# Optimization experiments

Hardware: AMD Instinct MI355X
Metric: run time of the kernel (lower is better)

Reference implementation:

```python
import jax, jax.numpy as jnp
import numpy as np

N0, N1, N2, N3 = 1_000_000, 200_000, 20_000, 2_048
E0, E1, E2 = 2_000_000, 200_000, 20_480
IN, HID, OUT = 128, 256, 47


def setup_inputs() -> dict:
    key = jax.random.key(0)
    ks = jax.random.split(key, 16)
    d = {}
    d["x"] = jax.random.normal(ks[0], (N0, IN), dtype=jnp.float32)
    # block edge lists (src index into layer-input nodes, dst into layer-output nodes)
    d["src0"] = jax.random.randint(ks[1], (E0,), 0, N0)
    d["dst0"] = jax.random.randint(ks[2], (E0,), 0, N1)
    d["src1"] = jax.random.randint(ks[3], (E1,), 0, N1)
    d["dst1"] = jax.random.randint(ks[4], (E1,), 0, N2)
    d["src2"] = jax.random.randint(ks[5], (E2,), 0, N2)
    d["dst2"] = jax.random.randint(ks[6], (E2,), 0, N3)
    # SAGEConv params: fc_self / fc_neigh (bias-free) + shared bias
    def lin(k, fi, fo):
        return jax.random.normal(k, (fi, fo), dtype=jnp.float32) / np.sqrt(fi).astype(np.float32)
    d["W_self0"], d["W_neigh0"], d["b0"] = lin(ks[7], IN, HID), lin(ks[8], IN, HID), jnp.zeros((HID,), jnp.float32)
    d["W_self1"], d["W_neigh1"], d["b1"] = lin(ks[9], HID, HID), lin(ks[10], HID, HID), jnp.zeros((HID,), jnp.float32)
    d["W_self2"], d["W_neigh2"], d["b2"] = lin(ks[11], HID, OUT), lin(ks[12], HID, OUT), jnp.zeros((OUT,), jnp.float32)
    return d


def _sage_layer(h, src, dst, n_dst, W_self, W_neigh, b):
    # gather messages from src nodes, mean-reduce onto dst nodes
    msg = h[src]                                   # [E, d_in]
    agg = jax.ops.segment_sum(msg, dst, num_segments=n_dst)
    deg = jax.ops.segment_sum(jnp.ones((src.shape[0],), h.dtype), dst, num_segments=n_dst)
    h_neigh = agg / jnp.maximum(deg, 1.0)[:, None]
    h_dst = h[:n_dst]                              # DGL block convention: dst = first n_dst src nodes
    return h_dst @ W_self + h_neigh @ W_neigh + b


def reference(x, src0, dst0, src1, dst1, src2, dst2,
              W_self0, W_neigh0, b0, W_self1, W_neigh1, b1, W_self2, W_neigh2, b2):
    h = _sage_layer(x, src0, dst0, N1, W_self0, W_neigh0, b0)
    h = jax.nn.relu(h)  # dropout is identity in eval mode
    h = _sage_layer(h, src1, dst1, N2, W_self1, W_neigh1, b1)
    h = jax.nn.relu(h)
    h = _sage_layer(h, src2, dst2, N3, W_self2, W_neigh2, b2)
    return h
```

## Files before the change

### kernel.cpp

```cpp
#include <hip/hip_runtime.h>

#define N0_ 1000000
#define N1_ 200000
#define N2_ 20000
#define N3_ 2048
#define E0_ 2000000
#define E1_ 200000
#define E2_ 20480
#define IN_ 128
#define HID_ 256
#define OUT_ 47

typedef unsigned short u16;
typedef unsigned int u32;
typedef __attribute__((ext_vector_type(8))) short b16x8;
typedef __attribute__((ext_vector_type(4))) float f32x4;
typedef __attribute__((ext_vector_type(4))) u16 u16x4;
typedef __attribute__((ext_vector_type(8))) u16 u16x8;

__device__ __forceinline__ u16 f2b(float f) {
  u32 u = __builtin_bit_cast(u32, f);
  return (u16)((u + 0x7FFFu + ((u >> 16) & 1u)) >> 16);
}
__device__ __forceinline__ float b2f(u16 b) {
  return __builtin_bit_cast(float, (u32)b << 16);
}

static constexpr size_t OFF_CNT  = 0;
static constexpr size_t OFF_CUR  = 200064;
static constexpr size_t OFF_RPTR = 400128;
static constexpr size_t OFF_BSUM = 600192;
static constexpr size_t OFF_EIDS = 600320;
static constexpr size_t OFF_BT0  = 2600320;
static constexpr size_t OFF_BT1  = 2633088;
static constexpr size_t OFF_HN0  = 2698624;
static constexpr size_t OFF_H1   = 15498624;
static constexpr size_t OFF_HN1  = 41098624;
static constexpr size_t OFF_H2   = 43658624;
static constexpr size_t OFF_HN2  = 46218624;

__global__ __launch_bounds__(256) void hist_kernel(const int* __restrict__ dst,
                                                   int* __restrict__ cnt, int nE) {
  int e = blockIdx.x * 256 + threadIdx.x;
  if (e < nE) atomicAdd(&cnt[dst[e]], 1);
}

__global__ __launch_bounds__(256) void scan_local(const int* __restrict__ in,
                                                  int* __restrict__ out,
                                                  int* __restrict__ bsum, int n) {
  __shared__ int s[256];
  const int b = blockIdx.x, t = threadIdx.x;
  const int base = b * 2048 + t * 8;
  int v[8];
  int sum = 0;
#pragma unroll
  for (int i = 0; i < 8; i++) {
    int idx = base + i;
    int x = (idx < n) ? in[idx] : 0;
    v[i] = sum;
    sum += x;
  }
  s[t] = sum;
  __syncthreads();
  for (int off = 1; off < 256; off <<= 1) {
    int x = 0;
    if (t >= off) x = s[t - off];
    __syncthreads();
    if (t >= off) s[t] += x;
    __syncthreads();
  }
  const int texcl = s[t] - sum;
#pragma unroll
  for (int i = 0; i < 8; i++) {
    int idx = base + i;
    if (idx < n) out[idx] = texcl + v[i];
  }
  if (t == 255) bsum[b] = s[255];
}

__global__ __launch_bounds__(256) void scan_add(int* __restrict__ rptr,
                                                const int* __restrict__ bsum,
                                                int n, int E) {
  const int b = blockIdx.x, t = threadIdx.x;
  int add = 0;
  for (int i = 0; i < b; i++) add += bsum[i];
  const int base = b * 2048 + t * 8;
#pragma unroll
  for (int i = 0; i < 8; i++) {
    int idx = base + i;
    if (idx < n) rptr[idx] += add;
  }
  if (b == 0 && t == 0) rptr[n] = E;
}

__global__ __launch_bounds__(256) void csr_fill(const int* __restrict__ src,
                                                const int* __restrict__ dst,
                                                const int* __restrict__ rptr,
                                                int* __restrict__ cursor,
                                                int* __restrict__ eids, int nE) {
  int e = blockIdx.x * 256 + threadIdx.x;
  if (e >= nE) return;
  int d = dst[e];
  int pos = rptr[d] + atomicAdd(&cursor[d], 1);
  eids[pos] = src[e];
}

__global__ __launch_bounds__(256) void pack_w(const float* __restrict__ Ws,
                                              const float* __restrict__ Wn,
                                              u16* __restrict__ Bt, int KS, int KT) {
  int t = blockIdx.x * 256 + threadIdx.x;
  if (t >= 256 * KT) return;
  int n = t & 255, k = t >> 8;
  float v = (k < KS) ? Ws[(size_t)k * 256 + n] : Wn[(size_t)(k - KS) * 256 + n];
  Bt[(size_t)n * KT + k] = f2b(v);
}

__global__ __launch_bounds__(256) void agg0(const float* __restrict__ h,
                                            const int* __restrict__ eids,
                                            const int* __restrict__ rptr,
                                            u16* __restrict__ out, int M) {
  int wid = (blockIdx.x * 256 + threadIdx.x) >> 6;
  int lane = threadIdx.x & 63;
  if (wid >= M) return;
  const int beg = rptr[wid], end = rptr[wid + 1];
  const int half = lane >> 5;
  const int col = (lane & 31) * 4;
  float a0 = 0.f, a1 = 0.f, a2 = 0.f, a3 = 0.f;
  for (int i = beg; i < end; i += 16) {
    int ids[8];
#pragma unroll
    for (int j = 0; j < 8; j++) {
      int idx = i + 2 * j + half;
      idx = idx < end ? idx : end - 1;
      ids[j] = eids[idx];
    }
    float4 v[8];
#pragma unroll
    for (int j = 0; j < 8; j++)
      v[j] = *reinterpret_cast<const float4*>(&h[(size_t)ids[j] * IN_ + col]);
#pragma unroll
    for (int j = 0; j < 8; j++) {
      if (i + 2 * j + half < end) {
        a0 += v[j].x; a1 += v[j].y; a2 += v[j].z; a3 += v[j].w;
      }
    }
  }
  a0 += __shfl_xor(a0, 32, 64);
  a1 += __shfl_xor(a1, 32, 64);
  a2 += __shfl_xor(a2, 32, 64);
  a3 += __shfl_xor(a3, 32, 64);
  if (half == 0) {
    float inv = 1.0f / fmaxf((float)(end - beg), 1.0f);
    u16x4 o;
    o[0] = f2b(a0 * inv); o[1] = f2b(a1 * inv);
    o[2] = f2b(a2 * inv); o[3] = f2b(a3 * inv);
    *reinterpret_cast<u16x4*>(&out[(size_t)wid * IN_ + col]) = o;
  }
}

__global__ __launch_bounds__(256) void agg1(const u16* __restrict__ h,
                                            const int* __restrict__ eids,
                                            const int* __restrict__ rptr,
                                            u16* __restrict__ out, int M) {
  int wid = (blockIdx.x * 256 + threadIdx.x) >> 6;
  int lane = threadIdx.x & 63;
  if (wid >= M) return;
  const int beg = rptr[wid], end = rptr[wid + 1];
  const int half = lane >> 5;
  const int col = (lane & 31) * 8;
  float a[8];
#pragma unroll
  for (int j = 0; j < 8; j++) a[j] = 0.f;
  for (int i = beg; i < end; i += 16) {
    int ids[8];
#pragma unroll
    for (int j = 0; j < 8; j++) {
      int idx = i + 2 * j + half;
      idx = idx < end ? idx : end - 1;
      ids[j] = eids[idx];
    }
    u16x8 v[8];
#pragma unroll
    for (int j = 0; j < 8; j++)
      v[j] = *reinterpret_cast<const u16x8*>(&h[(size_t)ids[j] * HID_ + col]);
#pragma unroll
    for (int j = 0; j < 8; j++) {
      if (i + 2 * j + half < end) {
#pragma unroll
        for (int c = 0; c < 8; c++) a[c] += b2f(v[j][c]);
      }
    }
  }
#pragma unroll
  for (int c = 0; c < 8; c++) a[c] += __shfl_xor(a[c], 32, 64);
  if (half == 0) {
    float inv = 1.0f / fmaxf((float)(end - beg), 1.0f);
    u16x8 o;
#pragma unroll
    for (int c = 0; c < 8; c++) o[c] = f2b(a[c] * inv);
    *reinterpret_cast<u16x8*>(&out[(size_t)wid * HID_ + col]) = o;
  }
}

template <int KSELF, bool A0F32>
__global__ __launch_bounds__(512) void sage_gemm_mfma(
    const void* __restrict__ A0v, const u16* __restrict__ A1,
    const u16* __restrict__ Bt, const float* __restrict__ bias,
    u16* __restrict__ outp, int M) {
  constexpr int KTOT = 2 * KSELF;
  __shared__ u16 As[128 * 64];
  __shared__ u16 Bs[256 * 64];
  const int tid = threadIdx.x;
  const int lane = tid & 63;
  const int w = tid >> 6;
  const int wm = w >> 2;
  const int wn = w & 3;
  const int m0 = blockIdx.x * 128;

  f32x4 acc[4][4];
#pragma unroll
  for (int m = 0; m < 4; m++)
#pragma unroll
    for (int n = 0; n < 4; n++) acc[m][n] = f32x4{0.f, 0.f, 0.f, 0.f};

  for (int kt = 0; kt < KTOT; kt += 64) {
    if (A0F32 && kt < KSELF) {
      const float* A0 = (const float*)A0v;
#pragma unroll
      for (int i = 0; i < 4; i++) {
        int e = tid + i * 512;
        int row = e >> 4;
        int c = (e & 15) * 4;
        int rowg = m0 + row; if (rowg >= M) rowg = M - 1;
        float4 v = *reinterpret_cast<const float4*>(&A0[(size_t)rowg * KSELF + kt + c]);
        u32 p0 = (u32)f2b(v.x) | ((u32)f2b(v.y) << 16);
        u32 p1 = (u32)f2b(v.z) | ((u32)f2b(v.w) << 16);
        int byt = ((row * 64 + c) * 2) ^ ((row & 7) << 4);
        u32* dp = reinterpret_cast<u32*>(reinterpret_cast<char*>(As) + byt);
        dp[0] = p0; dp[1] = p1;
      }
    } else {
      const u16* src; int ksrc;
      if (!A0F32 && kt < KSELF) { src = (const u16*)A0v; ksrc = kt; }
      else                      { src = A1;              ksrc = kt - KSELF; }
#pragma unroll
      for (int i = 0; i < 2; i++) {
        int e = tid + i * 512;
        int row = e >> 3;
        int ch = e & 7;
        int rowg = m0 + row; if (rowg >= M) rowg = M - 1;
        u16x8 v = *reinterpret_cast<const u16x8*>(&src[(size_t)rowg * KSELF + ksrc + ch * 8]);
        int byt = ((row * 64 + ch * 8) * 2) ^ ((row & 7) << 4);
        *reinterpret_cast<u16x8*>(reinterpret_cast<char*>(As) + byt) = v;
      }
    }
#pragma unroll
    for (int i = 0; i < 4; i++) {
      int e = tid + i * 512;
      int n = e >> 3;
      int ch = e & 7;
      u16x8 v = *reinterpret_cast<const u16x8*>(&Bt[(size_t)n * KTOT + kt + ch * 8]);
      int byt = ((n * 64 + ch * 8) * 2) ^ ((n & 7) << 4);
      *reinterpret_cast<u16x8*>(reinterpret_cast<char*>(Bs) + byt) = v;
    }
    __syncthreads();
#pragma unroll
    for (int kk = 0; kk < 64; kk += 32) {
      const int kb = (kk + (lane >> 4) * 8) * 2;
      b16x8 a[4], b[4];
#pragma unroll
      for (int m = 0; m < 4; m++) {
        int row = wm * 64 + m * 16 + (lane & 15);
        int byt = (row * 128 + kb) ^ ((row & 7) << 4);
        a[m] = *reinterpret_cast<const b16x8*>(reinterpret_cast<const char*>(As) + byt);
      }
#pragma unroll
      for (int n = 0; n < 4; n++) {
        int row = wn * 64 + n * 16 + (lane & 15);
        int byt = (row * 128 + kb) ^ ((row & 7) << 4);
        b[n] = *reinterpret_cast<const b16x8*>(reinterpret_cast<const char*>(Bs) + byt);
      }
#pragma unroll
      for (int m = 0; m < 4; m++)
#pragma unroll
        for (int n = 0; n < 4; n++)
          acc[m][n] = __builtin_amdgcn_mfma_f32_16x16x32_bf16(a[m], b[n], acc[m][n], 0, 0, 0);
    }
    __syncthreads();
  }
  float bv[4];
#pragma unroll
  for (int n = 0; n < 4; n++) bv[n] = bias[wn * 64 + n * 16 + (lane & 15)];
#pragma unroll
  for (int m = 0; m < 4; m++) {
    int rowb = m0 + wm * 64 + m * 16 + ((lane >> 4) << 2);
#pragma unroll
    for (int r = 0; r < 4; r++) {
      int row = rowb + r;
      if (row < M) {
#pragma unroll
        for (int n = 0; n < 4; n++) {
          float v = acc[m][n][r] + bv[n];
          v = fmaxf(v, 0.0f);
          outp[(size_t)row * 256 + wn * 64 + n * 16 + (lane & 15)] = f2b(v);
        }
      }
    }
  }
}

__global__ __launch_bounds__(64) void sage_gemm_out(
    const u16* __restrict__ h, const u16* __restrict__ hn,
    const float* __restrict__ Ws, const float* __restrict__ Wn,
    const float* __restrict__ bias, float* __restrict__ out) {
  __shared__ float As[512];
  const int row = blockIdx.x;
  const int t = threadIdx.x;
  u16x4 a = *reinterpret_cast<const u16x4*>(&h[(size_t)row * 256 + t * 4]);
  u16x4 b = *reinterpret_cast<const u16x4*>(&hn[(size_t)row * 256 + t * 4]);
#pragma unroll
  for (int j = 0; j < 4; j++) {
    As[t * 4 + j] = b2f(a[j]);
    As[256 + t * 4 + j] = b2f(b[j]);
  }
  __syncthreads();
  if (t < OUT_) {
    float s = bias[t];
#pragma unroll 8
    for (int k = 0; k < 256; k++) s = fmaf(As[k], Ws[k * 47 + t], s);
#pragma unroll 8
    for (int k = 0; k < 256; k++) s = fmaf(As[256 + k], Wn[k * 47 + t], s);
    out[(size_t)row * 47 + t] = s;
  }
}

static void build_csr(const int* src, const int* dst, int E, int M,
                      int* cnt, int* cursor, int* rptr, int* bsum, int* eids,
                      hipStream_t stream) {
  const int nb = (M + 2047) / 2048;
  hipMemsetAsync(cnt, 0, (size_t)(200064 + M) * 4, stream);
  hist_kernel<<<(E + 255) / 256, 256, 0, stream>>>(dst, cnt, E);
  scan_local<<<nb, 256, 0, stream>>>(cnt, rptr, bsum, M);
  scan_add<<<nb, 256, 0, stream>>>(rptr, bsum, M, E);
  csr_fill<<<(E + 255) / 256, 256, 0, stream>>>(src, dst, rptr, cursor, eids, E);
}

extern "C" void kernel_launch(void* const* d_in, const int* in_sizes, int n_in,
                              void* d_out, int out_size, void* d_ws, size_t ws_size,
                              hipStream_t stream) {
  const float* x      = (const float*)d_in[0];
  const int*   src0   = (const int*)d_in[1];
  const int*   dst0   = (const int*)d_in[2];
  const int*   src1   = (const int*)d_in[3];
  const int*   dst1   = (const int*)d_in[4];
  const int*   src2   = (const int*)d_in[5];
  const int*   dst2   = (const int*)d_in[6];
  const float* Wself0 = (const float*)d_in[7];
  const float* Wneigh0= (const float*)d_in[8];
  const float* b0     = (const float*)d_in[9];
  const float* Wself1 = (const float*)d_in[10];
  const float* Wneigh1= (const float*)d_in[11];
  const float* b1     = (const float*)d_in[12];
  const float* Wself2 = (const float*)d_in[13];
  const float* Wneigh2= (const float*)d_in[14];
  const float* b2     = (const float*)d_in[15];

  int* wsi   = (int*)d_ws;
  int* cnt   = wsi + OFF_CNT;
  int* cursor= wsi + OFF_CUR;
  int* rptr  = wsi + OFF_RPTR;
  int* bsum  = wsi + OFF_BSUM;
  int* eids  = wsi + OFF_EIDS;
  u16* Bt0   = (u16*)(wsi + OFF_BT0);
  u16* Bt1   = (u16*)(wsi + OFF_BT1);
  u16* HN0   = (u16*)(wsi + OFF_HN0);
  u16* H1    = (u16*)(wsi + OFF_H1);
  u16* HN1   = (u16*)(wsi + OFF_HN1);
  u16* H2    = (u16*)(wsi + OFF_H2);
  u16* HN2   = (u16*)(wsi + OFF_HN2);
  float* out = (float*)d_out;

  pack_w<<<(256 * 256 + 255) / 256, 256, 0, stream>>>(Wself0, Wneigh0, Bt0, IN_, 2 * IN_);
  pack_w<<<(256 * 512 + 255) / 256, 256, 0, stream>>>(Wself1, Wneigh1, Bt1, HID_, 2 * HID_);

  build_csr(src0, dst0, E0_, N1_, cnt, cursor, rptr, bsum, eids, stream);
  agg0<<<(N1_ + 3) / 4, 256, 0, stream>>>(x, eids, rptr, HN0, N1_);
  sage_gemm_mfma<IN_, true><<<(N1_ + 127) / 128, 512, 0, stream>>>(x, HN0, Bt0, b0, H1, N1_);

  build_csr(src1, dst1, E1_, N2_, cnt, cursor, rptr, bsum, eids, stream);
  agg1<<<(N2_ + 3) / 4, 256, 0, stream>>>(H1, eids, rptr, HN1, N2_);
  sage_gemm_mfma<HID_, false><<<(N2_ + 127) / 128, 512, 0, stream>>>(H1, HN1, Bt1, b1, H2, N2_);

  build_csr(src2, dst2, E2_, N3_, cnt, cursor, rptr, bsum, eids, stream);
  agg1<<<(N3_ + 3) / 4, 256, 0, stream>>>(H2, eids, rptr, HN2, N3_);
  sage_gemm_out<<<N3_, 64, 0, stream>>>(H2, HN2, Wself2, Wneigh2, b2, out);
}
```

Baseline: 561.4 us.

## Build all three CSRs at once and fuse aggregation into the layer GEMMs

All three layers' destination histograms, prefix scans and CSR fills now run as single combined launches over a concatenated node space, and the weight packing is folded into the histogram kernel. Layer 0's neighbour mean is computed straight into shared memory inside the MFMA GEMM kernel, so the bf16 HN0 buffer is never written to or read back from global memory. The final layer also aggregates neighbours inside the output kernel. This cuts launch count and global round trips, at the cost of a large shared-memory footprint and a serial aggregation phase before the GEMM in fused_sage0, which may lower occupancy and prevent overlap.

```diff
diff --git a/kernel.cpp b/kernel.cpp
--- a/kernel.cpp
+++ b/kernel.cpp
@@ -11,6 +11,9 @@
 #define HID_ 256
 #define OUT_ 47
 
+#define NTOT_ (N1_ + N2_ + N3_)
+#define ETOT_ (E0_ + E1_ + E2_)
+
 typedef unsigned short u16;
 typedef unsigned int u32;
 typedef __attribute__((ext_vector_type(8))) short b16x8;
@@ -27,22 +30,41 @@
 }
 
 static constexpr size_t OFF_CNT  = 0;
-static constexpr size_t OFF_CUR  = 200064;
-static constexpr size_t OFF_RPTR = 400128;
-static constexpr size_t OFF_BSUM = 600192;
-static constexpr size_t OFF_EIDS = 600320;
-static constexpr size_t OFF_BT0  = 2600320;
-static constexpr size_t OFF_BT1  = 2633088;
-static constexpr size_t OFF_HN0  = 2698624;
-static constexpr size_t OFF_H1   = 15498624;
-static constexpr size_t OFF_HN1  = 41098624;
-static constexpr size_t OFF_H2   = 43658624;
-static constexpr size_t OFF_HN2  = 46218624;
-
-__global__ __launch_bounds__(256) void hist_kernel(const int* __restrict__ dst,
-                                                   int* __restrict__ cnt, int nE) {
-  int e = blockIdx.x * 256 + threadIdx.x;
-  if (e < nE) atomicAdd(&cnt[dst[e]], 1);
+static constexpr size_t OFF_CUR  = 222048;
+static constexpr size_t OFF_RPTR = 444096;
+static constexpr size_t OFF_BSUM = 666176;
+static constexpr size_t OFF_EIDS = 666304;
+static constexpr size_t OFF_BT0  = 2886784;
+static constexpr size_t OFF_BT1  = 2919552;
+static constexpr size_t OFF_H1   = 2985088;
+static constexpr size_t OFF_HN1  = 28585088;
+static constexpr size_t OFF_H2   = 31145088;
+
+__global__ __launch_bounds__(256) void prep(
+    const int* __restrict__ dst0, const int* __restrict__ dst1,
+    const int* __restrict__ dst2,
+    const float* __restrict__ Ws0, const float* __restrict__ Wn0,
+    const float* __restrict__ Ws1, const float* __restrict__ Wn1,
+    int* __restrict__ cnt, u16* __restrict__ Bt0, u16* __restrict__ Bt1) {
+  int t = blockIdx.x * 256 + threadIdx.x;
+  if (t < E0_) { atomicAdd(&cnt[dst0[t]], 1); return; }
+  t -= E0_;
+  if (t < E1_) { atomicAdd(&cnt[N1_ + dst1[t]], 1); return; }
+  t -= E1_;
+  if (t < E2_) { atomicAdd(&cnt[N1_ + N2_ + dst2[t]], 1); return; }
+  t -= E2_;
+  if (t < 256 * 256) {
+    int n = t & 255, k = t >> 8;
+    float v = (k < IN_) ? Ws0[(size_t)k * 256 + n] : Wn0[(size_t)(k - IN_) * 256 + n];
+    Bt0[(size_t)n * 256 + k] = f2b(v);
+    return;
+  }
+  t -= 256 * 256;
+  if (t < 256 * 512) {
+    int n = t & 255, k = t >> 8;
+    float v = (k < HID_) ? Ws1[(size_t)k * 256 + n] : Wn1[(size_t)(k - HID_) * 256 + n];
+    Bt1[(size_t)n * 512 + k] = f2b(v);
+  }
 }
 
 __global__ __launch_bounds__(256) void scan_local(const int* __restrict__ in,
@@ -93,68 +115,159 @@
   if (b == 0 && t == 0) rptr[n] = E;
 }
 
-__global__ __launch_bounds__(256) void csr_fill(const int* __restrict__ src,
-                                                const int* __restrict__ dst,
-                                                const int* __restrict__ rptr,
-                                                int* __restrict__ cursor,
-                                                int* __restrict__ eids, int nE) {
+__global__ __launch_bounds__(256) void csr_fill_all(
+    const int* __restrict__ src0, const int* __restrict__ dst0,
+    const int* __restrict__ src1, const int* __restrict__ dst1,
+    const int* __restrict__ src2, const int* __restrict__ dst2,
+    const int* __restrict__ rptr, int* __restrict__ cursor,
+    int* __restrict__ eids) {
   int e = blockIdx.x * 256 + threadIdx.x;
-  if (e >= nE) return;
-  int d = dst[e];
-  int pos = rptr[d] + atomicAdd(&cursor[d], 1);
-  eids[pos] = src[e];
-}
-
-__global__ __launch_bounds__(256) void pack_w(const float* __restrict__ Ws,
-                                              const float* __restrict__ Wn,
-                                              u16* __restrict__ Bt, int KS, int KT) {
-  int t = blockIdx.x * 256 + threadIdx.x;
-  if (t >= 256 * KT) return;
-  int n = t & 255, k = t >> 8;
-  float v = (k < KS) ? Ws[(size_t)k * 256 + n] : Wn[(size_t)(k - KS) * 256 + n];
-  Bt[(size_t)n * KT + k] = f2b(v);
-}
-
-__global__ __launch_bounds__(256) void agg0(const float* __restrict__ h,
-                                            const int* __restrict__ eids,
-                                            const int* __restrict__ rptr,
-                                            u16* __restrict__ out, int M) {
-  int wid = (blockIdx.x * 256 + threadIdx.x) >> 6;
-  int lane = threadIdx.x & 63;
-  if (wid >= M) return;
-  const int beg = rptr[wid], end = rptr[wid + 1];
-  const int half = lane >> 5;
-  const int col = (lane & 31) * 4;
-  float a0 = 0.f, a1 = 0.f, a2 = 0.f, a3 = 0.f;
-  for (int i = beg; i < end; i += 16) {
-    int ids[8];
-#pragma unroll
-    for (int j = 0; j < 8; j++) {
-      int idx = i + 2 * j + half;
-      idx = idx < end ? idx : end - 1;
-      ids[j] = eids[idx];
-    }
-    float4 v[8];
-#pragma unroll
-    for (int j = 0; j < 8; j++)
-      v[j] = *reinterpret_cast<const float4*>(&h[(size_t)ids[j] * IN_ + col]);
-#pragma unroll
-    for (int j = 0; j < 8; j++) {
-      if (i + 2 * j + half < end) {
-        a0 += v[j].x; a1 += v[j].y; a2 += v[j].z; a3 += v[j].w;
-      }
-    }
-  }
-  a0 += __shfl_xor(a0, 32, 64);
-  a1 += __shfl_xor(a1, 32, 64);
-  a2 += __shfl_xor(a2, 32, 64);
-  a3 += __shfl_xor(a3, 32, 64);
-  if (half == 0) {
-    float inv = 1.0f / fmaxf((float)(end - beg), 1.0f);
-    u16x4 o;
-    o[0] = f2b(a0 * inv); o[1] = f2b(a1 * inv);
-    o[2] = f2b(a2 * inv); o[3] = f2b(a3 * inv);
-    *reinterpret_cast<u16x4*>(&out[(size_t)wid * IN_ + col]) = o;
+  int s, b;
+  if (e < E0_) { s = src0[e]; b = dst0[e]; }
+  else if (e < E0_ + E1_) { s = src1[e - E0_]; b = N1_ + dst1[e - E0_]; }
+  else if (e < ETOT_) { s = src2[e - E0_ - E1_]; b = N1_ + N2_ + dst2[e - E0_ - E1_]; }
+  else return;
+  int pos = rptr[b] + atomicAdd(&cursor[b], 1);
+  eids[pos] = s;
+}
+
+__global__ __launch_bounds__(512, 4) void fused_sage0(
+    const float* __restrict__ x, const int* __restrict__ eids,
+    const int* __restrict__ rptr, const u16* __restrict__ Bt,
+    const float* __restrict__ bias, u16* __restrict__ outp, int M) {
+  __shared__ u16 Bs[256 * 64];
+  __shared__ u16 As[128 * 64];
+  __shared__ u16 HN[128 * 128];
+  const int tid = threadIdx.x;
+  const int lane = tid & 63;
+  const int wv = tid >> 6;
+  const int m0 = blockIdx.x * 128;
+
+  {
+    const int half = lane >> 5;
+    const int colf = (lane & 31) * 4;
+    for (int r = 0; r < 16; r++) {
+      const int rl = wv * 16 + r;
+      int rowg = m0 + rl; if (rowg >= M) rowg = M - 1;
+      const int beg = rptr[rowg], end = rptr[rowg + 1];
+      float a0 = 0.f, a1 = 0.f, a2 = 0.f, a3 = 0.f;
+      for (int i = beg; i < end; i += 16) {
+        int ids[8];
+#pragma unroll
+        for (int j = 0; j < 8; j++) {
+          int idx = i + 2 * j + half;
+          idx = idx < end ? idx : end - 1;
+          ids[j] = eids[idx];
+        }
+        float4 v[8];
+#pragma unroll
+        for (int j = 0; j < 8; j++)
+          v[j] = *reinterpret_cast<const float4*>(&x[(size_t)ids[j] * IN_ + colf]);
+#pragma unroll
+        for (int j = 0; j < 8; j++) {
+          if (i + 2 * j + half < end) {
+            a0 += v[j].x; a1 += v[j].y; a2 += v[j].z; a3 += v[j].w;
+          }
+        }
+      }
+      a0 += __shfl_xor(a0, 32, 64);
+      a1 += __shfl_xor(a1, 32, 64);
+      a2 += __shfl_xor(a2, 32, 64);
+      a3 += __shfl_xor(a3, 32, 64);
+      if (half == 0) {
+        float inv = 1.0f / fmaxf((float)(end - beg), 1.0f);
+        u32 p0 = (u32)f2b(a0 * inv) | ((u32)f2b(a1 * inv) << 16);
+        u32 p1 = (u32)f2b(a2 * inv) | ((u32)f2b(a3 * inv) << 16);
+        int byt = (rl * 256 + colf * 2) ^ ((rl & 7) << 4);
+        u32* dp = reinterpret_cast<u32*>(reinterpret_cast<char*>(HN) + byt);
+        dp[0] = p0; dp[1] = p1;
+      }
+    }
+  }
+  __syncthreads();
+
+  const int wm = wv >> 2;
+  const int wn = wv & 3;
+  f32x4 acc[4][4];
+#pragma unroll
+  for (int m = 0; m < 4; m++)
+#pragma unroll
+    for (int n = 0; n < 4; n++) acc[m][n] = f32x4{0.f, 0.f, 0.f, 0.f};
+
+#pragma unroll
+  for (int kt = 0; kt < 256; kt += 64) {
+    if (kt < 128) {
+#pragma unroll
+      for (int i = 0; i < 4; i++) {
+        int e = tid + i * 512;
+        int row = e >> 4;
+        int c = (e & 15) * 4;
+        int rowg = m0 + row; if (rowg >= M) rowg = M - 1;
+        float4 v = *reinterpret_cast<const float4*>(&x[(size_t)rowg * IN_ + kt + c]);
+        u32 p0 = (u32)f2b(v.x) | ((u32)f2b(v.y) << 16);
+        u32 p1 = (u32)f2b(v.z) | ((u32)f2b(v.w) << 16);
+        int byt = ((row * 64 + c) * 2) ^ ((row & 7) << 4);
+        u32* dp = reinterpret_cast<u32*>(reinterpret_cast<char*>(As) + byt);
+        dp[0] = p0; dp[1] = p1;
+      }
+    }
+#pragma unroll
+    for (int i = 0; i < 4; i++) {
+      int e = tid + i * 512;
+      int n = e >> 3;
+      int ch = e & 7;
+      u16x8 v = *reinterpret_cast<const u16x8*>(&Bt[(size_t)n * 256 + kt + ch * 8]);
+      int byt = ((n * 64 + ch * 8) * 2) ^ ((n & 7) << 4);
+      *reinterpret_cast<u16x8*>(reinterpret_cast<char*>(Bs) + byt) = v;
+    }
+    __syncthreads();
+#pragma unroll
+    for (int kk = 0; kk < 64; kk += 32) {
+      const int ksl = kk + (lane >> 4) * 8;
+      b16x8 a[4], b[4];
+#pragma unroll
+      for (int m = 0; m < 4; m++) {
+        int row = wm * 64 + m * 16 + (lane & 15);
+        if (kt < 128) {
+          int byt = (row * 128 + ksl * 2) ^ ((row & 7) << 4);
+          a[m] = *reinterpret_cast<const b16x8*>(reinterpret_cast<const char*>(As) + byt);
+        } else {
+          int byt = (row * 256 + (kt - 128 + ksl) * 2) ^ ((row & 7) << 4);
+          a[m] = *reinterpret_cast<const b16x8*>(reinterpret_cast<const char*>(HN) + byt);
+        }
+      }
+#pragma unroll
+      for (int n = 0; n < 4; n++) {
+        int row = wn * 64 + n * 16 + (lane & 15);
+        int byt = (row * 128 + ksl * 2) ^ ((row & 7) << 4);
+        b[n] = *reinterpret_cast<const b16x8*>(reinterpret_cast<const char*>(Bs) + byt);
+      }
+#pragma unroll
+      for (int m = 0; m < 4; m++)
+#pragma unroll
+        for (int n = 0; n < 4; n++)
+          acc[m][n] = __builtin_amdgcn_mfma_f32_16x16x32_bf16(a[m], b[n], acc[m][n], 0, 0, 0);
+    }
+    __syncthreads();
+  }
+  float bv[4];
+#pragma unroll
+  for (int n = 0; n < 4; n++) bv[n] = bias[wn * 64 + n * 16 + (lane & 15)];
+#pragma unroll
+  for (int m = 0; m < 4; m++) {
+    int rowb = m0 + wm * 64 + m * 16 + ((lane >> 4) << 2);
+#pragma unroll
+    for (int r = 0; r < 4; r++) {
+      int row = rowb + r;
+      if (row < M) {
+#pragma unroll
+        for (int n = 0; n < 4; n++) {
+          float v = acc[m][n][r] + bv[n];
+          v = fmaxf(v, 0.0f);
+          outp[(size_t)row * 256 + wn * 64 + n * 16 + (lane & 15)] = f2b(v);
+        }
+      }
+    }
   }
 }
 
@@ -202,9 +315,9 @@
   }
 }
 
-template <int KSELF, bool A0F32>
+template <int KSELF>
 __global__ __launch_bounds__(512) void sage_gemm_mfma(
-    const void* __restrict__ A0v, const u16* __restrict__ A1,
+    const u16* __restrict__ A0, const u16* __restrict__ A1,
     const u16* __restrict__ Bt, const float* __restrict__ bias,
     u16* __restrict__ outp, int M) {
   constexpr int KTOT = 2 * KSELF;
@@ -224,35 +337,18 @@
     for (int n = 0; n < 4; n++) acc[m][n] = f32x4{0.f, 0.f, 0.f, 0.f};
 
   for (int kt = 0; kt < KTOT; kt += 64) {
-    if (A0F32 && kt < KSELF) {
-      const float* A0 = (const float*)A0v;
-#pragma unroll
-      for (int i = 0; i < 4; i++) {
-        int e = tid + i * 512;
-        int row = e >> 4;
-        int c = (e & 15) * 4;
-        int rowg = m0 + row; if (rowg >= M) rowg = M - 1;
-        float4 v = *reinterpret_cast<const float4*>(&A0[(size_t)rowg * KSELF + kt + c]);
-        u32 p0 = (u32)f2b(v.x) | ((u32)f2b(v.y) << 16);
-        u32 p1 = (u32)f2b(v.z) | ((u32)f2b(v.w) << 16);
-        int byt = ((row * 64 + c) * 2) ^ ((row & 7) << 4);
-        u32* dp = reinterpret_cast<u32*>(reinterpret_cast<char*>(As) + byt);
-        dp[0] = p0; dp[1] = p1;
-      }
-    } else {
-      const u16* src; int ksrc;
-      if (!A0F32 && kt < KSELF) { src = (const u16*)A0v; ksrc = kt; }
-      else                      { src = A1;              ksrc = kt - KSELF; }
-#pragma unroll
-      for (int i = 0; i < 2; i++) {
-        int e = tid + i * 512;
-        int row = e >> 3;
-        int ch = e & 7;
-        int rowg = m0 + row; if (rowg >= M) rowg = M - 1;
-        u16x8 v = *reinterpret_cast<const u16x8*>(&src[(size_t)rowg * KSELF + ksrc + ch * 8]);
-        int byt = ((row * 64 + ch * 8) * 2) ^ ((row & 7) << 4);
-        *reinterpret_cast<u16x8*>(reinterpret_cast<char*>(As) + byt) = v;
-      }
+    const u16* src; int ksrc;
+    if (kt < KSELF) { src = A0; ksrc = kt; }
+    else            { src = A1; ksrc = kt - KSELF; }
+#pragma unroll
+    for (int i = 0; i < 2; i++) {
+      int e = tid + i * 512;
+      int row = e >> 3;
+      int ch = e & 7;
+      int rowg = m0 + row; if (rowg >= M) rowg = M - 1;
+      u16x8 v = *reinterpret_cast<const u16x8*>(&src[(size_t)rowg * KSELF + ksrc + ch * 8]);
+      int byt = ((row * 64 + ch * 8) * 2) ^ ((row & 7) << 4);
+      *reinterpret_cast<u16x8*>(reinterpret_cast<char*>(As) + byt) = v;
     }
 #pragma unroll
     for (int i = 0; i < 4; i++) {
@@ -309,20 +405,38 @@
   }
 }
 
-__global__ __launch_bounds__(64) void sage_gemm_out(
-    const u16* __restrict__ h, const u16* __restrict__ hn,
-    const float* __restrict__ Ws, const float* __restrict__ Wn,
-    const float* __restrict__ bias, float* __restrict__ out) {
+__global__ __launch_bounds__(64) void fused_out(
+    const u16* __restrict__ h, const int* __restrict__ eids,
+    const int* __restrict__ rptr, const float* __restrict__ Ws,
+    const float* __restrict__ Wn, const float* __restrict__ bias,
+    float* __restrict__ out) {
   __shared__ float As[512];
   const int row = blockIdx.x;
   const int t = threadIdx.x;
   u16x4 a = *reinterpret_cast<const u16x4*>(&h[(size_t)row * 256 + t * 4]);
-  u16x4 b = *reinterpret_cast<const u16x4*>(&hn[(size_t)row * 256 + t * 4]);
-#pragma unroll
-  for (int j = 0; j < 4; j++) {
-    As[t * 4 + j] = b2f(a[j]);
-    As[256 + t * 4 + j] = b2f(b[j]);
-  }
+#pragma unroll
+  for (int j = 0; j < 4; j++) As[t * 4 + j] = b2f(a[j]);
+  const int beg = rptr[row], end = rptr[row + 1];
+  float s0 = 0.f, s1 = 0.f, s2 = 0.f, s3 = 0.f;
+  for (int i = beg; i < end; i += 4) {
+    int i1 = (i + 1 < end) ? i + 1 : i;
+    int i2 = (i + 2 < end) ? i + 2 : i;
+    int i3 = (i + 3 < end) ? i + 3 : i;
+    int e0 = eids[i], e1 = eids[i1], e2 = eids[i2], e3 = eids[i3];
+    u16x4 v0 = *reinterpret_cast<const u16x4*>(&h[(size_t)e0 * 256 + t * 4]);
+    u16x4 v1 = *reinterpret_cast<const u16x4*>(&h[(size_t)e1 * 256 + t * 4]);
+    u16x4 v2 = *reinterpret_cast<const u16x4*>(&h[(size_t)e2 * 256 + t * 4]);
+    u16x4 v3 = *reinterpret_cast<const u16x4*>(&h[(size_t)e3 * 256 + t * 4]);
+    s0 += b2f(v0[0]); s1 += b2f(v0[1]); s2 += b2f(v0[2]); s3 += b2f(v0[3]);
+    if (i + 1 < end) { s0 += b2f(v1[0]); s1 += b2f(v1[1]); s2 += b2f(v1[2]); s3 += b2f(v1[3]); }
+    if (i + 2 < end) { s0 += b2f(v2[0]); s1 += b2f(v2[1]); s2 += b2f(v2[2]); s3 += b2f(v2[3]); }
+    if (i + 3 < end) { s0 += b2f(v3[0]); s1 += b2f(v3[1]); s2 += b2f(v3[2]); s3 += b2f(v3[3]); }
+  }
+  float inv = 1.0f / fmaxf((float)(end - beg), 1.0f);
+  As[256 + t * 4 + 0] = s0 * inv;
+  As[256 + t * 4 + 1] = s1 * inv;
+  As[256 + t * 4 + 2] = s2 * inv;
+  As[256 + t * 4 + 3] = s3 * inv;
   __syncthreads();
   if (t < OUT_) {
     float s = bias[t];
@@ -332,17 +446,6 @@
     for (int k = 0; k < 256; k++) s = fmaf(As[256 + k], Wn[k * 47 + t], s);
     out[(size_t)row * 47 + t] = s;
   }
-}
-
-static void build_csr(const int* src, const int* dst, int E, int M,
-                      int* cnt, int* cursor, int* rptr, int* bsum, int* eids,
-                      hipStream_t stream) {
-  const int nb = (M + 2047) / 2048;
-  hipMemsetAsync(cnt, 0, (size_t)(200064 + M) * 4, stream);
-  hist_kernel<<<(E + 255) / 256, 256, 0, stream>>>(dst, cnt, E);
-  scan_local<<<nb, 256, 0, stream>>>(cnt, rptr, bsum, M);
-  scan_add<<<nb, 256, 0, stream>>>(rptr, bsum, M, E);
-  csr_fill<<<(E + 255) / 256, 256, 0, stream>>>(src, dst, rptr, cursor, eids, E);
 }
 
 extern "C" void kernel_launch(void* const* d_in, const int* in_sizes, int n_in,
@@ -373,25 +476,30 @@
   int* eids  = wsi + OFF_EIDS;
   u16* Bt0   = (u16*)(wsi + OFF_BT0);
   u16* Bt1   = (u16*)(wsi + OFF_BT1);
-  u16* HN0   = (u16*)(wsi + OFF_HN0);
   u16* H1    = (u16*)(wsi + OFF_H1);
   u16* HN1   = (u16*)(wsi + OFF_HN1);
   u16* H2    = (u16*)(wsi + OFF_H2);
-  u16* HN2   = (u16*)(wsi + OFF_HN2);
   float* out = (float*)d_out;
 
-  pack_w<<<(256 * 256 + 255) / 256, 256, 0, stream>>>(Wself0, Wneigh0, Bt0, IN_, 2 * IN_);
-  pack_w<<<(256 * 512 + 255) / 256, 256, 0, stream>>>(Wself1, Wneigh1, Bt1, HID_, 2 * HID_);
-
-  build_csr(src0, dst0, E0_, N1_, cnt, cursor, rptr, bsum, eids, stream);
-  agg0<<<(N1_ + 3) / 4, 256, 0, stream>>>(x, eids, rptr, HN0, N1_);
-  sage_gemm_mfma<IN_, true><<<(N1_ + 127) / 128, 512, 0, stream>>>(x, HN0, Bt0, b0, H1, N1_);
-
-  build_csr(src1, dst1, E1_, N2_, cnt, cursor, rptr, bsum, eids, stream);
-  agg1<<<(N2_ + 3) / 4, 256, 0, stream>>>(H1, eids, rptr, HN1, N2_);
-  sage_gemm_mfma<HID_, false><<<(N2_ + 127) / 128, 512, 0, stream>>>(H1, HN1, Bt1, b1, H2, N2_);
-
-  build_csr(src2, dst2, E2_, N3_, cnt, cursor, rptr, bsum, eids, stream);
-  agg1<<<(N3_ + 3) / 4, 256, 0, stream>>>(H2, eids, rptr, HN2, N3_);
-  sage_gemm_out<<<N3_, 64, 0, stream>>>(H2, HN2, Wself2, Wneigh2, b2, out);
-}
+  hipMemsetAsync(cnt, 0, (size_t)(2 * NTOT_) * 4, stream);
+
+  {
+    int total = ETOT_ + 256 * 256 + 256 * 512;
+    prep<<<(total + 255) / 256, 256, 0, stream>>>(
+        dst0, dst1, dst2, Wself0, Wneigh0, Wself1, Wneigh1, cnt, Bt0, Bt1);
+  }
+  {
+    const int nb = (NTOT_ + 2047) / 2048;
+    scan_local<<<nb, 256, 0, stream>>>(cnt, rptr, bsum, NTOT_);
+    scan_add<<<nb, 256, 0, stream>>>(rptr, bsum, NTOT_, ETOT_);
+    csr_fill_all<<<(ETOT_ + 255) / 256, 256, 0, stream>>>(
+        src0, dst0, src1, dst1, src2, dst2, rptr, cursor, eids);
+  }
+
+  fused_sage0<<<(N1_ + 127) / 128, 512, 0, stream>>>(x, eids, rptr, Bt0, b0, H1, N1_);
+
+  agg1<<<(N2_ + 3) / 4, 256, 0, stream>>>(H1, eids, rptr + N1_, HN1, N2_);
+  sage_gemm_mfma<HID_><<<(N2_ + 127) / 128, 512, 0, stream>>>(H1, HN1, Bt1, b1, H2, N2_);
+
+  fused_out<<<N3_, 64, 0, stream>>>(H2, eids, rptr + N1_ + N2_, Wself2, Wneigh2, b2, out);
+}
```

Result: slower. 580.4 us (+3.4%).
